# Kernel tuning notes

Measured on AMD Instinct MI355X. Metric: run time of the kernel, lower is better.

## Reference

```python
import jax, jax.numpy as jnp
import numpy as np

D_MODEL = 1024


def setup_inputs() -> dict:
    key = jax.random.key(0)
    ks = jax.random.split(key, 9)
    B, S, D = 4, 2048, D_MODEL
    scale = 1.0 / np.sqrt(D)
    inp = {
        "tokens": jax.random.normal(ks[0], (B, S, D), dtype=jnp.float32),
        "Wq": jax.random.normal(ks[1], (D, D), dtype=jnp.float32) * scale,
        "bq": jnp.zeros((D,), dtype=jnp.float32),
        "Wk": jax.random.normal(ks[2], (D, D), dtype=jnp.float32) * scale,
        "bk": jnp.zeros((D,), dtype=jnp.float32),
        "Wv": jax.random.normal(ks[3], (D, D), dtype=jnp.float32) * scale,
        "bv": jnp.zeros((D,), dtype=jnp.float32),
        "Wo": jax.random.normal(ks[4], (D, D), dtype=jnp.float32) * scale,
        "bo": jnp.zeros((D,), dtype=jnp.float32),
    }
    return inp


def reference(tokens, Wq, bq, Wk, bk, Wv, bv, Wo, bo):
    # use_activation=True, use_residual=True
    residual = tokens
    x = jax.nn.gelu(tokens, approximate=False)  # F.gelu default is exact (erf)
    q = jnp.einsum("bsd,de->bse", x, Wq) + bq
    k = jnp.einsum("bsd,de->bse", x, Wk) + bk
    v = jnp.einsum("bsd,de->bse", x, Wv) + bv
    scale = 1.0 / jnp.sqrt(jnp.asarray(tokens.shape[-1], dtype=tokens.dtype))
    scores = jnp.einsum("bqd,bkd->bqk", q, k) * scale  # [B,S,S]
    attn = jax.nn.softmax(scores, axis=-1)
    mixed = jnp.einsum("bqk,bkd->bqd", attn, v)
    out = jnp.einsum("bsd,de->bse", mixed, Wo) + bo
    return out + residual
```

## Files before the change

kernel.cpp:

```cpp
#include <hip/hip_runtime.h>
#include <hip/hip_bf16.h>
#include <cstdint>
#include <cstddef>

typedef unsigned short u16;
using frag_ab = __attribute__((ext_vector_type(8))) short;
using f32x4   = __attribute__((ext_vector_type(4))) float;

__device__ __forceinline__ u16 f2bf(float x) {
    __hip_bfloat16 h = __float2bfloat16(x);
    return *reinterpret_cast<u16*>(&h);
}

__device__ __forceinline__ void gload_lds16(const u16* g, u16* l) {
    __builtin_amdgcn_global_load_lds(
        (const __attribute__((address_space(1))) uint32_t*)g,
        (__attribute__((address_space(3)))       uint32_t*)l,
        16, 0, 0);
}

#define WAITV4() do { asm volatile("s_waitcnt vmcnt(4)" ::: "memory"); \
                      __builtin_amdgcn_sched_barrier(0); } while (0)
#define WAITV0() do { asm volatile("s_waitcnt vmcnt(0)" ::: "memory"); \
                      __builtin_amdgcn_sched_barrier(0); } while (0)
#define BAR()    do { asm volatile("" ::: "memory"); __builtin_amdgcn_s_barrier(); \
                      __builtin_amdgcn_sched_barrier(0); } while (0)
#define LGKMC(N) do { asm volatile("s_waitcnt lgkmcnt(" #N ")" ::: "memory"); \
                      __builtin_amdgcn_sched_barrier(0); } while (0)
#define LGKM0()  LGKMC(0)

template<int EPI, int BN_>
__global__ __launch_bounds__(512, 2)
void gemm8p(const u16* __restrict__ A, const u16* __restrict__ Bt,
            void* __restrict__ C0,
            const float* __restrict__ b0, const float* __restrict__ resid,
            int K, int lda, int ldb, int ldc,
            long long sA, long long sB, long long sC, float alpha,
            float* __restrict__ partials)
{
    constexpr int NFQ    = BN_ / 64;
    constexpr int WN     = BN_ / 2;
    constexpr int BUFSTR = 16384 + BN_ * 64;
    __shared__ __align__(16) u16 lds[2 * BUFSTR];

    const int z = blockIdx.z;
    A  += (long long)z * sA;
    Bt += (long long)z * sB;

    const int gx  = gridDim.x;
    const int nwg = gx * gridDim.y;
    const int cpx = nwg >> 3;
    int lin = blockIdx.x + gx * blockIdx.y;
    lin = (lin & 7) * cpx + (lin >> 3);
    const int m0 = (lin / gx) * 256;
    const int n0 = (lin % gx) * BN_;

    const int t    = threadIdx.x;
    const int lane = t & 63;
    const int wave = t >> 6;
    const int wm   = wave >> 1;
    const int wn   = wave & 1;

    const int r0  = t >> 3;
    const int ssw = (t & 7) ^ (r0 & 7);
    const u16* gsA0_0 = A  + (size_t)(m0 +       r0) * lda + ssw * 8;
    const u16* gsA0_1 = A  + (size_t)(m0 +  64 + r0) * lda + ssw * 8;
    const u16* gsA1_0 = A  + (size_t)(m0 + 128 + r0) * lda + ssw * 8;
    const u16* gsA1_1 = A  + (size_t)(m0 + 192 + r0) * lda + ssw * 8;
    const u16* gsB0_0 = Bt + (size_t)(n0 +       r0) * ldb + ssw * 8;
    const u16* gsB0_1 = Bt + (size_t)(n0 +  64 + r0) * ldb + ssw * 8;
    const u16* gsB1_0 = (BN_ == 256) ? Bt + (size_t)(n0 + 128 + r0) * ldb + ssw * 8 : gsB0_0;
    const u16* gsB1_1 = (BN_ == 256) ? Bt + (size_t)(n0 + 192 + r0) * ldb + ssw * 8 : gsB0_1;

#define OPO_A 0
#define OPO_B 16384
#define STAGE(BI, OP, H, KT) do {                                              \
    gload_lds16(gs##OP##H##_0 + (size_t)(KT) * 64,                             \
                lds + (BI) * BUFSTR + OPO_##OP + (H) * 8192 + t * 8);          \
    gload_lds16(gs##OP##H##_1 + (size_t)(KT) * 64,                             \
                lds + (BI) * BUFSTR + OPO_##OP + (H) * 8192 + 4096 + t * 8);   \
} while (0)

    const int ar   = lane & 15;
    const int ko   = lane >> 4;
    const int aoff = (wm * 64 + ar) * 64;
    const int boff = OPO_B + (wn * WN + ar) * 64;
    const int as0  = ((0 + ko) ^ (ar & 7)) * 8;
    const int as1  = ((4 + ko) ^ (ar & 7)) * 8;

    frag_ab areg[2][2];
    frag_ab breg[2][NFQ][2];
    f32x4   acc[4][2 * NFQ] = {};

#define RDA(BI, MQ) do { _Pragma("unroll") for (int mf = 0; mf < 2; ++mf) {    \
    areg[mf][0] = *(const frag_ab*)(lds + (BI)*BUFSTR + aoff + ((MQ)*2+mf)*1024 + as0); \
    areg[mf][1] = *(const frag_ab*)(lds + (BI)*BUFSTR + aoff + ((MQ)*2+mf)*1024 + as1); } } while (0)

#define RDB(BI, NQ) do { _Pragma("unroll") for (int jf = 0; jf < NFQ; ++jf) {  \
    breg[NQ][jf][0] = *(const frag_ab*)(lds + (BI)*BUFSTR + boff + ((NQ)*NFQ+jf)*1024 + as0); \
    breg[NQ][jf][1] = *(const frag_ab*)(lds + (BI)*BUFSTR + boff + ((NQ)*NFQ+jf)*1024 + as1); } } while (0)

#define MMAQ(MQ, NQ) do { __builtin_amdgcn_s_setprio(1);                       \
    _Pragma("unroll") for (int mf = 0; mf < 2; ++mf)                           \
    _Pragma("unroll") for (int jf = 0; jf < NFQ; ++jf) {                       \
        acc[(MQ)*2+mf][(NQ)*NFQ+jf] = __builtin_amdgcn_mfma_f32_16x16x32_bf16( \
            areg[mf][0], breg[NQ][jf][0], acc[(MQ)*2+mf][(NQ)*NFQ+jf], 0,0,0); \
        acc[(MQ)*2+mf][(NQ)*NFQ+jf] = __builtin_amdgcn_mfma_f32_16x16x32_bf16( \
            areg[mf][1], breg[NQ][jf][1], acc[(MQ)*2+mf][(NQ)*NFQ+jf], 0,0,0); \
    } __builtin_amdgcn_s_setprio(0); } while (0)

    const int nk = K / 64;
    STAGE(0, A, 0, 0); STAGE(0, A, 1, 0); STAGE(0, B, 0, 0);
    if constexpr (BN_ == 256) STAGE(0, B, 1, 0);
    STAGE(1, B, 0, 1); STAGE(1, A, 0, 1);
    WAITV4();
    BAR();

    const int nIter = nk >> 1;
    for (int it = 0; it < nIter; ++it) {
        const int O  = 2 * it + 1;
        const int E2 = (2 * it + 2 < nk) ? 2 * it + 2 : nk - 1;
        const int O2 = (2 * it + 3 < nk) ? 2 * it + 3 : nk - 1;

        RDA(0, 0); RDB(0, 0);
        STAGE(1, A, 1, O);
        if constexpr (BN_ == 256) LGKMC(8);
        BAR(); LGKM0(); MMAQ(0, 0);
        RDB(0, 1);
        if constexpr (BN_ == 256) STAGE(1, B, 1, O);
        BAR(); LGKM0(); MMAQ(0, 1);
        RDA(0, 1);
        STAGE(0, B, 0, E2);
        BAR(); LGKM0(); MMAQ(1, 0);
        STAGE(0, A, 0, E2);
        WAITV4();
        BAR(); MMAQ(1, 1);
        RDA(1, 0); RDB(1, 0);
        STAGE(0, A, 1, E2);
        if constexpr (BN_ == 256) LGKMC(8);
        BAR(); LGKM0(); MMAQ(0, 0);
        RDB(1, 1);
        if constexpr (BN_ == 256) STAGE(0, B, 1, E2);
        BAR(); LGKM0(); MMAQ(0, 1);
        RDA(1, 1);
        STAGE(1, B, 0, O2);
        BAR(); LGKM0(); MMAQ(1, 0);
        STAGE(1, A, 0, O2);
        WAITV4();
        BAR(); MMAQ(1, 1);
    }

    const int cr = (lane >> 4) * 4;
    const int cc = lane & 15;

    float* fl = (float*)lds;
    if constexpr (EPI == 2) {
        WAITV0();
        BAR();
        if (t < 256) {
            const float* p = partials + ((size_t)z * 2048 + m0 + t) * 16;
            float s = 0.0f;
            #pragma unroll
            for (int i = 0; i < 16; ++i) s += p[i];
            fl[t] = 1.0f / s;
        }
        BAR();
    }

    float rs[4][4];
    if constexpr (EPI == 1) {
        #pragma unroll
        for (int mi = 0; mi < 4; ++mi)
            #pragma unroll
            for (int r = 0; r < 4; ++r) rs[mi][r] = 0.0f;
    }

    #pragma unroll
    for (int mi = 0; mi < 4; ++mi) {
        const int rowb = m0 + wm * 64 + mi * 16 + cr;
        const int rloc = wm * 64 + mi * 16 + cr;
        #pragma unroll
        for (int gj = 0; gj < 2 * NFQ; ++gj) {
            const int col = n0 + wn * WN + gj * 16 + cc;
            const float bvv = (EPI == 3) ? b0[col] : 0.0f;
            #pragma unroll
            for (int r = 0; r < 4; ++r) {
                const size_t row = (size_t)(rowb + r);
                float v = acc[mi][gj][r];
                if (EPI == 1) { v = __expf(v * alpha); rs[mi][r] += v; }
                if (EPI == 2) v *= fl[rloc + r];
                v += bvv;
                if (EPI == 3) {
                    v += resid[row * ldc + col];
                    ((float*)C0)[(size_t)z * sC + row * ldc + col] = v;
                } else {
                    ((u16*)C0)[(size_t)z * sC + row * ldc + col] = f2bf(v);
                }
            }
        }
    }

    if constexpr (EPI == 1) {
        #pragma unroll
        for (int mi = 0; mi < 4; ++mi)
            #pragma unroll
            for (int r = 0; r < 4; ++r) {
                float s = rs[mi][r];
                s += __shfl_xor(s, 1); s += __shfl_xor(s, 2);
                s += __shfl_xor(s, 4); s += __shfl_xor(s, 8);
                rs[mi][r] = s;
            }
        if (cc == 0) {
            const int chunk = (n0 >> 7) + wn;
            #pragma unroll
            for (int mi = 0; mi < 4; ++mi) {
                const int rowb = m0 + wm * 64 + mi * 16 + cr;
                #pragma unroll
                for (int r = 0; r < 4; ++r)
                    partials[((size_t)z * 2048 + rowb + r) * 16 + chunk] = rs[mi][r];
            }
        }
    }
#undef STAGE
#undef RDA
#undef RDB
#undef MMAQ
#undef OPO_A
#undef OPO_B
}

__global__ __launch_bounds__(512, 2)
void gemmQK3(const u16* __restrict__ A, const u16* __restrict__ Bt,
             u16* __restrict__ C0, const float* __restrict__ b0,
             const float* __restrict__ b1,
             int K, int lda, int ldb, int ldc, long long sC)
{
    __shared__ __align__(16) u16 lds[81920];

    const int gx  = gridDim.x;
    const int nwg = gx * gridDim.y;
    const int cpx = nwg >> 3;
    int lin = blockIdx.x + gx * blockIdx.y;
    lin = (lin & 7) * cpx + (lin >> 3);
    const int m0 = (lin / gx) * 256;
    const int n0 = (lin % gx) * 256;

    const int t    = threadIdx.x;
    const int lane = t & 63;
    const int wave = t >> 6;
    const int wm   = wave >> 1;
    const int wn   = wave & 1;

    const int r0  = t >> 3;
    const int ssw = (t & 7) ^ (r0 & 7);
    const u16* gsA_0 = A  + (size_t)(m0 +       r0) * lda + ssw * 8;
    const u16* gsA_1 = A  + (size_t)(m0 +  64 + r0) * lda + ssw * 8;
    const u16* gsA_2 = A  + (size_t)(m0 + 128 + r0) * lda + ssw * 8;
    const u16* gsA_3 = A  + (size_t)(m0 + 192 + r0) * lda + ssw * 8;
    const u16* gsB_0 = Bt + (size_t)(n0 +       r0) * ldb + ssw * 8;
    const u16* gsB_1 = Bt + (size_t)(n0 +  64 + r0) * ldb + ssw * 8;
    const u16* gsB_2 = Bt + (size_t)(n0 + 128 + r0) * ldb + ssw * 8;
    const u16* gsB_3 = Bt + (size_t)(n0 + 192 + r0) * ldb + ssw * 8;

#define STA(BUF, H, KT) do {                                                   \
    gload_lds16(((H) ? gsA_2 : gsA_0) + (size_t)(KT) * 64,                     \
                lds + (BUF) * 16384 + (H) * 8192 + t * 8);                     \
    gload_lds16(((H) ? gsA_3 : gsA_1) + (size_t)(KT) * 64,                     \
                lds + (BUF) * 16384 + (H) * 8192 + 4096 + t * 8);              \
} while (0)
#define STB(BUF, H, KT) do {                                                   \
    gload_lds16(((H) ? gsB_2 : gsB_0) + (size_t)(KT) * 64,                     \
                lds + 49152 + (BUF) * 16384 + (H) * 8192 + t * 8);             \
    gload_lds16(((H) ? gsB_3 : gsB_1) + (size_t)(KT) * 64,                     \
                lds + 49152 + (BUF) * 16384 + (H) * 8192 + 4096 + t * 8);      \
} while (0)

    const int ar   = lane & 15;
    const int ko   = lane >> 4;
    const int aoff = (wm * 64 + ar) * 64;
    const int boff = 49152 + (wn * 128 + ar) * 64;
    const int as0  = ((0 + ko) ^ (ar & 7)) * 8;
    const int as1  = ((4 + ko) ^ (ar & 7)) * 8;

    frag_ab areg[2][2];
    frag_ab breg[2][4][2];
    f32x4   acc[4][8] = {};

#define RDA3(AB, MQ) do { _Pragma("unroll") for (int mf = 0; mf < 2; ++mf) {   \
    areg[mf][0] = *(const frag_ab*)(lds + (AB) + aoff + ((MQ)*2+mf)*1024 + as0); \
    areg[mf][1] = *(const frag_ab*)(lds + (AB) + aoff + ((MQ)*2+mf)*1024 + as1); } } while (0)

#define RDB3(BB, NQ) do { _Pragma("unroll") for (int jf = 0; jf < 4; ++jf) {   \
    breg[NQ][jf][0] = *(const frag_ab*)(lds + (BB) + boff + ((NQ)*4+jf)*1024 + as0); \
    breg[NQ][jf][1] = *(const frag_ab*)(lds + (BB) + boff + ((NQ)*4+jf)*1024 + as1); } } while (0)

#define MMAQ3(MQ, NQ) do { __builtin_amdgcn_s_setprio(1);                      \
    _Pragma("unroll") for (int mf = 0; mf < 2; ++mf)                           \
    _Pragma("unroll") for (int jf = 0; jf < 4; ++jf) {                         \
        acc[(MQ)*2+mf][(NQ)*4+jf] = __builtin_amdgcn_mfma_f32_16x16x32_bf16(   \
            areg[mf][0], breg[NQ][jf][0], acc[(MQ)*2+mf][(NQ)*4+jf], 0,0,0);   \
        acc[(MQ)*2+mf][(NQ)*4+jf] = __builtin_amdgcn_mfma_f32_16x16x32_bf16(   \
            areg[mf][1], breg[NQ][jf][1], acc[(MQ)*2+mf][(NQ)*4+jf], 0,0,0);   \
    } __builtin_amdgcn_s_setprio(0); } while (0)

    const int nk = K / 64;
    STA(0, 0, 0); STA(0, 1, 0);
    STB(0, 0, 0); STB(0, 1, 0);
    STA(1, 0, 1); STA(1, 1, 1);
    WAITV4();
    BAR();

    int ab = 0, bb = 0;
    for (int tt = 0; tt < nk; ++tt) {
        const int ab2 = (ab + 2 >= 3) ? ab - 1 : ab + 2;
        const int bb1 = bb ^ 1;
        const int tB  = (tt + 1 < nk) ? tt + 1 : nk - 1;
        const int tA  = (tt + 2 < nk) ? tt + 2 : nk - 1;
        const int AB = ab * 16384, BB = bb * 16384;
        RDA3(AB, 0); RDB3(BB, 0);
        STB(bb1, 0, tB);
        LGKMC(8);
        BAR(); LGKM0(); MMAQ3(0, 0);
        RDB3(BB, 1);
        STB(bb1, 1, tB);
        BAR(); LGKM0(); MMAQ3(0, 1);
        RDA3(AB, 1);
        STA(ab2, 0, tA);
        BAR(); LGKM0(); MMAQ3(1, 0);
        STA(ab2, 1, tA);
        WAITV4();
        BAR(); MMAQ3(1, 1);
        ab = (ab + 1 >= 3) ? 0 : ab + 1;
        bb = bb1;
    }

    const int cr = (lane >> 4) * 4;
    const int cc = lane & 15;
    #pragma unroll
    for (int mi = 0; mi < 4; ++mi) {
        const int rowb = m0 + wm * 64 + mi * 16 + cr;
        #pragma unroll
        for (int gj = 0; gj < 8; ++gj) {
            const int col = n0 + wn * 128 + gj * 16 + cc;
            const int plane = col >> 10;
            const int cl    = col & 1023;
            const float bvv = ((plane == 0) ? b0 : b1)[cl];
            u16* Cw = C0 + (size_t)plane * sC;
            #pragma unroll
            for (int r = 0; r < 4; ++r)
                Cw[(size_t)(rowb + r) * ldc + cl] = f2bf(acc[mi][gj][r] + bvv);
        }
    }
#undef STA
#undef STB
#undef RDA3
#undef RDB3
#undef MMAQ3
}

__global__ __launch_bounds__(256, 2)
void gemm128_v(const u16* __restrict__ A, const u16* __restrict__ Bt,
               u16* __restrict__ VT, const float* __restrict__ bv,
               int K, int lda, int ldb)
{
    constexpr int BUFSTR = 16384;
    __shared__ __align__(16) u16 lds[2 * BUFSTR];

    const int gx  = gridDim.x;
    const int nwg = gx * gridDim.y;
    const int cpx = nwg >> 3;
    int lin = blockIdx.x + gx * blockIdx.y;
    lin = (lin & 7) * cpx + (lin >> 3);
    const int m0 = (lin / gx) * 128;
    const int n0 = (lin % gx) * 128;

    const int t    = threadIdx.x;
    const int lane = t & 63;
    const int wave = t >> 6;
    const int wm   = wave >> 1;
    const int wn   = wave & 1;

    const int r0  = t >> 3;
    const int ssw = (t & 7) ^ (r0 & 7);
    const u16* gsA0_0 = A  + (size_t)(m0 +       r0) * lda + ssw * 8;
    const u16* gsA0_1 = A  + (size_t)(m0 +  32 + r0) * lda + ssw * 8;
    const u16* gsA1_0 = A  + (size_t)(m0 +  64 + r0) * lda + ssw * 8;
    const u16* gsA1_1 = A  + (size_t)(m0 +  96 + r0) * lda + ssw * 8;
    const u16* gsB0_0 = Bt + (size_t)(n0 +       r0) * ldb + ssw * 8;
    const u16* gsB0_1 = Bt + (size_t)(n0 +  32 + r0) * ldb + ssw * 8;
    const u16* gsB1_0 = Bt + (size_t)(n0 +  64 + r0) * ldb + ssw * 8;
    const u16* gsB1_1 = Bt + (size_t)(n0 +  96 + r0) * ldb + ssw * 8;

#define OPO_A 0
#define OPO_B 8192
#define STAGE(BI, OP, H, KT) do {                                              \
    gload_lds16(gs##OP##H##_0 + (size_t)(KT) * 64,                             \
                lds + (BI) * BUFSTR + OPO_##OP + (H) * 4096 + t * 8);          \
    gload_lds16(gs##OP##H##_1 + (size_t)(KT) * 64,                             \
                lds + (BI) * BUFSTR + OPO_##OP + (H) * 4096 + 2048 + t * 8);   \
} while (0)

    const int ar   = lane & 15;
    const int ko   = lane >> 4;
    const int aoff = (wm * 64 + ar) * 64;
    const int boff = OPO_B + (wn * 64 + ar) * 64;
    const int as0  = ((0 + ko) ^ (ar & 7)) * 8;
    const int as1  = ((4 + ko) ^ (ar & 7)) * 8;

    frag_ab areg[2][2];
    frag_ab breg[2][2][2];
    f32x4   acc[4][4] = {};

#define RDA(BI, MQ) do { _Pragma("unroll") for (int mf = 0; mf < 2; ++mf) {    \
    areg[mf][0] = *(const frag_ab*)(lds + (BI)*BUFSTR + aoff + ((MQ)*2+mf)*1024 + as0); \
    areg[mf][1] = *(const frag_ab*)(lds + (BI)*BUFSTR + aoff + ((MQ)*2+mf)*1024 + as1); } } while (0)

#define RDB(BI, NQ) do { _Pragma("unroll") for (int jf = 0; jf < 2; ++jf) {    \
    breg[NQ][jf][0] = *(const frag_ab*)(lds + (BI)*BUFSTR + boff + ((NQ)*2+jf)*1024 + as0); \
    breg[NQ][jf][1] = *(const frag_ab*)(lds + (BI)*BUFSTR + boff + ((NQ)*2+jf)*1024 + as1); } } while (0)

#define MMAQ(MQ, NQ) do { __builtin_amdgcn_s_setprio(1);                       \
    _Pragma("unroll") for (int mf = 0; mf < 2; ++mf)                           \
    _Pragma("unroll") for (int jf = 0; jf < 2; ++jf) {                         \
        acc[(MQ)*2+mf][(NQ)*2+jf] = __builtin_amdgcn_mfma_f32_16x16x32_bf16(   \
            areg[mf][0], breg[NQ][jf][0], acc[(MQ)*2+mf][(NQ)*2+jf], 0,0,0);   \
        acc[(MQ)*2+mf][(NQ)*2+jf] = __builtin_amdgcn_mfma_f32_16x16x32_bf16(   \
            areg[mf][1], breg[NQ][jf][1], acc[(MQ)*2+mf][(NQ)*2+jf], 0,0,0);   \
    } __builtin_amdgcn_s_setprio(0); } while (0)

    const int nk = K / 64;
    STAGE(0, A, 0, 0); STAGE(0, A, 1, 0); STAGE(0, B, 0, 0); STAGE(0, B, 1, 0);
    STAGE(1, B, 0, 1); STAGE(1, A, 0, 1);
    WAITV4();
    BAR();

    const int nIter = nk >> 1;
    for (int it = 0; it < nIter; ++it) {
        const int O  = 2 * it + 1;
        const int E2 = (2 * it + 2 < nk) ? 2 * it + 2 : nk - 1;
        const int O2 = (2 * it + 3 < nk) ? 2 * it + 3 : nk - 1;

        RDA(0, 0); RDB(0, 0); STAGE(1, A, 1, O);  BAR(); LGKM0(); MMAQ(0, 0);
        RDB(0, 1);            STAGE(1, B, 1, O);  BAR(); LGKM0(); MMAQ(0, 1);
        RDA(0, 1);            STAGE(0, B, 0, E2); BAR(); LGKM0(); MMAQ(1, 0);
        STAGE(0, A, 0, E2);   WAITV4();           BAR();          MMAQ(1, 1);
        RDA(1, 0); RDB(1, 0); STAGE(0, A, 1, E2); BAR(); LGKM0(); MMAQ(0, 0);
        RDB(1, 1);            STAGE(0, B, 1, E2); BAR(); LGKM0(); MMAQ(0, 1);
        RDA(1, 1);            STAGE(1, B, 0, O2); BAR(); LGKM0(); MMAQ(1, 0);
        STAGE(1, A, 0, O2);   WAITV4();           BAR();          MMAQ(1, 1);
    }

    const int cr = (lane >> 4) * 4;
    const int cc = lane & 15;

    WAITV0();
    BAR();
    constexpr int TP = 136;
    u16* T = lds;
    #pragma unroll
    for (int mi = 0; mi < 4; ++mi) {
        const int rloc = wm * 64 + mi * 16 + cr;
        #pragma unroll
        for (int gj = 0; gj < 4; ++gj) {
            const int cl = wn * 64 + gj * 16 + cc;
            const float bvv = bv[n0 + cl];
            union { u16 u[4]; uint2 q; } pk;
            #pragma unroll
            for (int r = 0; r < 4; ++r) pk.u[r] = f2bf(acc[mi][gj][r] + bvv);
            *(uint2*)&T[cl * TP + rloc] = pk.q;
        }
    }
    BAR();
    const int bb   = m0 >> 11;
    const int s0   = m0 & 2047;
    const int d    = t >> 1;
    const int half = t & 1;
    const u16* src = T + d * TP + half * 64;
    u16* dg = VT + (size_t)bb * 1024 * 2048 + (size_t)(n0 + d) * 2048 + s0 + half * 64;
    #pragma unroll
    for (int j = 0; j < 8; ++j)
        ((uint4*)dg)[j] = ((const uint4*)src)[j];
#undef STAGE
#undef RDA
#undef RDB
#undef MMAQ
#undef OPO_A
#undef OPO_B
}

__global__ __launch_bounds__(256)
void prep_kernel(const float4* __restrict__ in, uint4* __restrict__ outp,
                 const float* __restrict__ W0, const float* __restrict__ W1,
                 const float* __restrict__ W2, const float* __restrict__ W3,
                 u16* __restrict__ WT, int D, int NG)
{
    __shared__ float tile[32][33];
    const int b = blockIdx.x;
    const int t = threadIdx.x;
    if (b < NG) {
        const int i = (b * 256 + t) * 2;
        float4 x0 = in[i], x1 = in[i + 1];
        auto g = [](float v) { return 0.5f * v * (1.0f + erff(v * 0.70710678118654752f)); };
        union { u16 u[8]; uint4 q; } pk;
        pk.u[0] = f2bf(g(x0.x)); pk.u[1] = f2bf(g(x0.y));
        pk.u[2] = f2bf(g(x0.z)); pk.u[3] = f2bf(g(x0.w));
        pk.u[4] = f2bf(g(x1.x)); pk.u[5] = f2bf(g(x1.y));
        pk.u[6] = f2bf(g(x1.z)); pk.u[7] = f2bf(g(x1.w));
        outp[b * 256 + t] = pk.q;
        return;
    }
    const int j   = b - NG;
    const int z   = j >> 10;
    const int rem = j & 1023;
    const int n0  = (rem & 31) * 32;
    const int k0  = (rem >> 5) * 32;
    const float* W = (z == 0) ? W0 : (z == 1) ? W1 : (z == 2) ? W2 : W3;
    u16* o = WT + (size_t)z * D * D;
    const int tx = t & 31, ty = t >> 5;
    #pragma unroll
    for (int r = 0; r < 4; ++r)
        tile[ty + 8 * r][tx] = W[(size_t)(k0 + ty + 8 * r) * D + n0 + tx];
    __syncthreads();
    #pragma unroll
    for (int r = 0; r < 4; ++r)
        o[(size_t)(n0 + ty + 8 * r) * D + k0 + tx] = f2bf(tile[tx][ty + 8 * r]);
}

extern "C" void kernel_launch(void* const* d_in, const int* in_sizes, int n_in,
                              void* d_out, int out_size, void* d_ws, size_t ws_size,
                              hipStream_t stream)
{
    const int B = 4, S = 2048, D = 1024;
    const int M = B * S;

    const float* tokens = (const float*)d_in[0];
    const float* Wq = (const float*)d_in[1];
    const float* bq = (const float*)d_in[2];
    const float* Wk = (const float*)d_in[3];
    const float* bk = (const float*)d_in[4];
    const float* Wv = (const float*)d_in[5];
    const float* bv = (const float*)d_in[6];
    const float* Wo = (const float*)d_in[7];
    const float* bo = (const float*)d_in[8];
    float* out = (float*)d_out;

    char* ws = (char*)d_ws;
    size_t o = 0;
    u16* x_bf = (u16*)(ws + o); o += (size_t)M * D * 2;
    u16* wT   = (u16*)(ws + o); o += (size_t)4 * D * D * 2;
    u16* q_bf = (u16*)(ws + o); o += (size_t)M * D * 2;
    u16* k_bf = (u16*)(ws + o); o += (size_t)M * D * 2;
    u16* vt   = (u16*)(ws + o); o += (size_t)M * D * 2;
    u16*   E        = (u16*)(ws + o);   o += (size_t)B * S * S * 2;
    float* partials = (float*)(ws + o); o += (size_t)B * S * 16 * 4;
    u16* mixed = x_bf;

    const int NG = M * D / 8 / 256;
    prep_kernel<<<dim3(NG + 4096), dim3(256), 0, stream>>>(
        (const float4*)tokens, (uint4*)x_bf, Wq, Wk, Wv, Wo, wT, D, NG);

    gemmQK3<<<dim3(2 * D / 256, M / 256, 1), dim3(512), 0, stream>>>(
        x_bf, wT, q_bf, bq, bk, D, D, D, D, (long long)M * D);

    gemm128_v<<<dim3(D / 128, M / 128, 1), dim3(256), 0, stream>>>(
        x_bf, wT + 2 * D * D, vt, bv, D, D, D);

    gemm8p<1, 256><<<dim3(S / 256, S / 256, B), dim3(512), 0, stream>>>(
        q_bf, k_bf, E, nullptr, nullptr,
        D, D, D, S, (long long)S * D, (long long)S * D, (long long)S * S, 0.03125f,
        partials);

    gemm8p<2, 128><<<dim3(D / 128, S / 256, B), dim3(512), 0, stream>>>(
        E, vt, mixed, nullptr, nullptr,
        S, S, S, D, (long long)S * S, (long long)D * S, (long long)S * D, 1.0f,
        partials);

    gemm8p<3, 128><<<dim3(D / 128, M / 256, 1), dim3(512), 0, stream>>>(
        mixed, wT + 3 * D * D, out, bo, tokens,
        D, D, D, D, 0, 0, 0, 1.0f, nullptr);
}
```

Measured before the change: 168.3 us.

## Unify GEMMs on triple-buffered A / double-buffered B pipeline kernel

Replaces the double-buffered gemm8p main loop with the gemmQK3-style schedule, which uses three A buffers and two B buffers so A tiles are prefetched two k-steps ahead. The QK projection, the scores GEMM, the PV GEMM and the output projection all use this one templated kernel, with the QK bias split handled as a new epilogue mode. This aims to hide more global load latency per k-step. The cost is more LDS per block, which may reduce occupancy, particularly for the BN=256 variants. The weight transpose in prep also now writes packed 32-bit pairs instead of 16-bit scalars, for wider coalesced stores.

```diff
diff --git a/kernel.cpp b/kernel.cpp
--- a/kernel.cpp
+++ b/kernel.cpp
@@ -31,17 +31,17 @@
 
 template<int EPI, int BN_>
 __global__ __launch_bounds__(512, 2)
-void gemm8p(const u16* __restrict__ A, const u16* __restrict__ Bt,
+void gemm3a(const u16* __restrict__ A, const u16* __restrict__ Bt,
             void* __restrict__ C0,
             const float* __restrict__ b0, const float* __restrict__ resid,
             int K, int lda, int ldb, int ldc,
             long long sA, long long sB, long long sC, float alpha,
             float* __restrict__ partials)
 {
-    constexpr int NFQ    = BN_ / 64;
-    constexpr int WN     = BN_ / 2;
-    constexpr int BUFSTR = 16384 + BN_ * 64;
-    __shared__ __align__(16) u16 lds[2 * BUFSTR];
+    constexpr int NFQ  = BN_ / 64;
+    constexpr int WN   = BN_ / 2;
+    constexpr int BBUF = BN_ * 64;
+    __shared__ __align__(16) u16 lds[49152 + 2 * BBUF];
 
     const int z = blockIdx.z;
     A  += (long long)z * sA;
@@ -63,28 +63,32 @@
 
     const int r0  = t >> 3;
     const int ssw = (t & 7) ^ (r0 & 7);
-    const u16* gsA0_0 = A  + (size_t)(m0 +       r0) * lda + ssw * 8;
-    const u16* gsA0_1 = A  + (size_t)(m0 +  64 + r0) * lda + ssw * 8;
-    const u16* gsA1_0 = A  + (size_t)(m0 + 128 + r0) * lda + ssw * 8;
-    const u16* gsA1_1 = A  + (size_t)(m0 + 192 + r0) * lda + ssw * 8;
-    const u16* gsB0_0 = Bt + (size_t)(n0 +       r0) * ldb + ssw * 8;
-    const u16* gsB0_1 = Bt + (size_t)(n0 +  64 + r0) * ldb + ssw * 8;
-    const u16* gsB1_0 = (BN_ == 256) ? Bt + (size_t)(n0 + 128 + r0) * ldb + ssw * 8 : gsB0_0;
-    const u16* gsB1_1 = (BN_ == 256) ? Bt + (size_t)(n0 + 192 + r0) * ldb + ssw * 8 : gsB0_1;
-
-#define OPO_A 0
-#define OPO_B 16384
-#define STAGE(BI, OP, H, KT) do {                                              \
-    gload_lds16(gs##OP##H##_0 + (size_t)(KT) * 64,                             \
-                lds + (BI) * BUFSTR + OPO_##OP + (H) * 8192 + t * 8);          \
-    gload_lds16(gs##OP##H##_1 + (size_t)(KT) * 64,                             \
-                lds + (BI) * BUFSTR + OPO_##OP + (H) * 8192 + 4096 + t * 8);   \
+    const u16* gsA_0 = A  + (size_t)(m0 +       r0) * lda + ssw * 8;
+    const u16* gsA_1 = A  + (size_t)(m0 +  64 + r0) * lda + ssw * 8;
+    const u16* gsA_2 = A  + (size_t)(m0 + 128 + r0) * lda + ssw * 8;
+    const u16* gsA_3 = A  + (size_t)(m0 + 192 + r0) * lda + ssw * 8;
+    const u16* gsB_0 = Bt + (size_t)(n0 +       r0) * ldb + ssw * 8;
+    const u16* gsB_1 = Bt + (size_t)(n0 +  64 + r0) * ldb + ssw * 8;
+    const u16* gsB_2 = (BN_ == 256) ? Bt + (size_t)(n0 + 128 + r0) * ldb + ssw * 8 : gsB_0;
+    const u16* gsB_3 = (BN_ == 256) ? Bt + (size_t)(n0 + 192 + r0) * ldb + ssw * 8 : gsB_1;
+
+#define STA(BUF, H, KT) do {                                                   \
+    gload_lds16(((H) ? gsA_2 : gsA_0) + (size_t)(KT) * 64,                     \
+                lds + (BUF) * 16384 + (H) * 8192 + t * 8);                     \
+    gload_lds16(((H) ? gsA_3 : gsA_1) + (size_t)(KT) * 64,                     \
+                lds + (BUF) * 16384 + (H) * 8192 + 4096 + t * 8);              \
+} while (0)
+#define STB(BUF, H, KT) do {                                                   \
+    gload_lds16(((H) ? gsB_2 : gsB_0) + (size_t)(KT) * 64,                     \
+                lds + 49152 + (BUF) * BBUF + (H) * 8192 + t * 8);              \
+    gload_lds16(((H) ? gsB_3 : gsB_1) + (size_t)(KT) * 64,                     \
+                lds + 49152 + (BUF) * BBUF + (H) * 8192 + 4096 + t * 8);       \
 } while (0)
 
     const int ar   = lane & 15;
     const int ko   = lane >> 4;
     const int aoff = (wm * 64 + ar) * 64;
-    const int boff = OPO_B + (wn * WN + ar) * 64;
+    const int boff = 49152 + (wn * WN + ar) * 64;
     const int as0  = ((0 + ko) ^ (ar & 7)) * 8;
     const int as1  = ((4 + ko) ^ (ar & 7)) * 8;
 
@@ -92,15 +96,15 @@
     frag_ab breg[2][NFQ][2];
     f32x4   acc[4][2 * NFQ] = {};
 
-#define RDA(BI, MQ) do { _Pragma("unroll") for (int mf = 0; mf < 2; ++mf) {    \
-    areg[mf][0] = *(const frag_ab*)(lds + (BI)*BUFSTR + aoff + ((MQ)*2+mf)*1024 + as0); \
-    areg[mf][1] = *(const frag_ab*)(lds + (BI)*BUFSTR + aoff + ((MQ)*2+mf)*1024 + as1); } } while (0)
-
-#define RDB(BI, NQ) do { _Pragma("unroll") for (int jf = 0; jf < NFQ; ++jf) {  \
-    breg[NQ][jf][0] = *(const frag_ab*)(lds + (BI)*BUFSTR + boff + ((NQ)*NFQ+jf)*1024 + as0); \
-    breg[NQ][jf][1] = *(const frag_ab*)(lds + (BI)*BUFSTR + boff + ((NQ)*NFQ+jf)*1024 + as1); } } while (0)
-
-#define MMAQ(MQ, NQ) do { __builtin_amdgcn_s_setprio(1);                       \
+#define RDA3(AB, MQ) do { _Pragma("unroll") for (int mf = 0; mf < 2; ++mf) {   \
+    areg[mf][0] = *(const frag_ab*)(lds + (AB) + aoff + ((MQ)*2+mf)*1024 + as0); \
+    areg[mf][1] = *(const frag_ab*)(lds + (AB) + aoff + ((MQ)*2+mf)*1024 + as1); } } while (0)
+
+#define RDB3(BO, NQ) do { _Pragma("unroll") for (int jf = 0; jf < NFQ; ++jf) { \
+    breg[NQ][jf][0] = *(const frag_ab*)(lds + (BO) + boff + ((NQ)*NFQ+jf)*1024 + as0); \
+    breg[NQ][jf][1] = *(const frag_ab*)(lds + (BO) + boff + ((NQ)*NFQ+jf)*1024 + as1); } } while (0)
+
+#define MMAQ3(MQ, NQ) do { __builtin_amdgcn_s_setprio(1);                      \
     _Pragma("unroll") for (int mf = 0; mf < 2; ++mf)                           \
     _Pragma("unroll") for (int jf = 0; jf < NFQ; ++jf) {                       \
         acc[(MQ)*2+mf][(NQ)*NFQ+jf] = __builtin_amdgcn_mfma_f32_16x16x32_bf16( \
@@ -110,44 +114,35 @@
     } __builtin_amdgcn_s_setprio(0); } while (0)
 
     const int nk = K / 64;
-    STAGE(0, A, 0, 0); STAGE(0, A, 1, 0); STAGE(0, B, 0, 0);
-    if constexpr (BN_ == 256) STAGE(0, B, 1, 0);
-    STAGE(1, B, 0, 1); STAGE(1, A, 0, 1);
+    STA(0, 0, 0); STA(0, 1, 0);
+    STB(0, 0, 0);
+    if constexpr (BN_ == 256) STB(0, 1, 0);
+    STA(1, 0, 1); STA(1, 1, 1);
     WAITV4();
     BAR();
 
-    const int nIter = nk >> 1;
-    for (int it = 0; it < nIter; ++it) {
-        const int O  = 2 * it + 1;
-        const int E2 = (2 * it + 2 < nk) ? 2 * it + 2 : nk - 1;
-        const int O2 = (2 * it + 3 < nk) ? 2 * it + 3 : nk - 1;
-
-        RDA(0, 0); RDB(0, 0);
-        STAGE(1, A, 1, O);
+    int ab = 0, bb = 0;
+    for (int tt = 0; tt < nk; ++tt) {
+        const int ab2 = (ab + 2 >= 3) ? ab - 1 : ab + 2;
+        const int bb1 = bb ^ 1;
+        const int tB  = (tt + 1 < nk) ? tt + 1 : nk - 1;
+        const int tA  = (tt + 2 < nk) ? tt + 2 : nk - 1;
+        const int AB = ab * 16384, BB = bb * BBUF;
+        RDA3(AB, 0); RDB3(BB, 0);
+        STB(bb1, 0, tB);
         if constexpr (BN_ == 256) LGKMC(8);
-        BAR(); LGKM0(); MMAQ(0, 0);
-        RDB(0, 1);
-        if constexpr (BN_ == 256) STAGE(1, B, 1, O);
-        BAR(); LGKM0(); MMAQ(0, 1);
-        RDA(0, 1);
-        STAGE(0, B, 0, E2);
-        BAR(); LGKM0(); MMAQ(1, 0);
-        STAGE(0, A, 0, E2);
+        BAR(); LGKM0(); MMAQ3(0, 0);
+        RDB3(BB, 1);
+        if constexpr (BN_ == 256) STB(bb1, 1, tB);
+        BAR(); LGKM0(); MMAQ3(0, 1);
+        RDA3(AB, 1);
+        STA(ab2, 0, tA);
+        BAR(); LGKM0(); MMAQ3(1, 0);
+        STA(ab2, 1, tA);
         WAITV4();
-        BAR(); MMAQ(1, 1);
-        RDA(1, 0); RDB(1, 0);
-        STAGE(0, A, 1, E2);
-        if constexpr (BN_ == 256) LGKMC(8);
-        BAR(); LGKM0(); MMAQ(0, 0);
-        RDB(1, 1);
-        if constexpr (BN_ == 256) STAGE(0, B, 1, E2);
-        BAR(); LGKM0(); MMAQ(0, 1);
-        RDA(1, 1);
-        STAGE(1, B, 0, O2);
-        BAR(); LGKM0(); MMAQ(1, 0);
-        STAGE(1, A, 0, O2);
-        WAITV4();
-        BAR(); MMAQ(1, 1);
+        BAR(); MMAQ3(1, 1);
+        ab = (ab + 1 >= 3) ? 0 : ab + 1;
+        bb = bb1;
     }
 
     const int cr = (lane >> 4) * 4;
@@ -182,19 +177,29 @@
         #pragma unroll
         for (int gj = 0; gj < 2 * NFQ; ++gj) {
             const int col = n0 + wn * WN + gj * 16 + cc;
-            const float bvv = (EPI == 3) ? b0[col] : 0.0f;
-            #pragma unroll
-            for (int r = 0; r < 4; ++r) {
-                const size_t row = (size_t)(rowb + r);
-                float v = acc[mi][gj][r];
-                if (EPI == 1) { v = __expf(v * alpha); rs[mi][r] += v; }
-                if (EPI == 2) v *= fl[rloc + r];
-                v += bvv;
-                if (EPI == 3) {
-                    v += resid[row * ldc + col];
-                    ((float*)C0)[(size_t)z * sC + row * ldc + col] = v;
-                } else {
-                    ((u16*)C0)[(size_t)z * sC + row * ldc + col] = f2bf(v);
+            if constexpr (EPI == 0) {
+                const int plane = col >> 10;
+                const int cl    = col & 1023;
+                const float bvv = ((plane == 0) ? b0 : resid)[cl];
+                u16* Cw = (u16*)C0 + (size_t)plane * sC;
+                #pragma unroll
+                for (int r = 0; r < 4; ++r)
+                    Cw[(size_t)(rowb + r) * ldc + cl] = f2bf(acc[mi][gj][r] + bvv);
+            } else {
+                const float bvv = (EPI == 3) ? b0[col] : 0.0f;
+                #pragma unroll
+                for (int r = 0; r < 4; ++r) {
+                    const size_t row = (size_t)(rowb + r);
+                    float v = acc[mi][gj][r];
+                    if (EPI == 1) { v = __expf(v * alpha); rs[mi][r] += v; }
+                    if (EPI == 2) v *= fl[rloc + r];
+                    v += bvv;
+                    if (EPI == 3) {
+                        v += resid[row * ldc + col];
+                        ((float*)C0)[(size_t)z * sC + row * ldc + col] = v;
+                    } else {
+                        ((u16*)C0)[(size_t)z * sC + row * ldc + col] = f2bf(v);
+                    }
                 }
             }
         }
@@ -221,136 +226,6 @@
             }
         }
     }
-#undef STAGE
-#undef RDA
-#undef RDB
-#undef MMAQ
-#undef OPO_A
-#undef OPO_B
-}
-
-__global__ __launch_bounds__(512, 2)
-void gemmQK3(const u16* __restrict__ A, const u16* __restrict__ Bt,
-             u16* __restrict__ C0, const float* __restrict__ b0,
-             const float* __restrict__ b1,
-             int K, int lda, int ldb, int ldc, long long sC)
-{
-    __shared__ __align__(16) u16 lds[81920];
-
-    const int gx  = gridDim.x;
-    const int nwg = gx * gridDim.y;
-    const int cpx = nwg >> 3;
-    int lin = blockIdx.x + gx * blockIdx.y;
-    lin = (lin & 7) * cpx + (lin >> 3);
-    const int m0 = (lin / gx) * 256;
-    const int n0 = (lin % gx) * 256;
-
-    const int t    = threadIdx.x;
-    const int lane = t & 63;
-    const int wave = t >> 6;
-    const int wm   = wave >> 1;
-    const int wn   = wave & 1;
-
-    const int r0  = t >> 3;
-    const int ssw = (t & 7) ^ (r0 & 7);
-    const u16* gsA_0 = A  + (size_t)(m0 +       r0) * lda + ssw * 8;
-    const u16* gsA_1 = A  + (size_t)(m0 +  64 + r0) * lda + ssw * 8;
-    const u16* gsA_2 = A  + (size_t)(m0 + 128 + r0) * lda + ssw * 8;
-    const u16* gsA_3 = A  + (size_t)(m0 + 192 + r0) * lda + ssw * 8;
-    const u16* gsB_0 = Bt + (size_t)(n0 +       r0) * ldb + ssw * 8;
-    const u16* gsB_1 = Bt + (size_t)(n0 +  64 + r0) * ldb + ssw * 8;
-    const u16* gsB_2 = Bt + (size_t)(n0 + 128 + r0) * ldb + ssw * 8;
-    const u16* gsB_3 = Bt + (size_t)(n0 + 192 + r0) * ldb + ssw * 8;
-
-#define STA(BUF, H, KT) do {                                                   \
-    gload_lds16(((H) ? gsA_2 : gsA_0) + (size_t)(KT) * 64,                     \
-                lds + (BUF) * 16384 + (H) * 8192 + t * 8);                     \
-    gload_lds16(((H) ? gsA_3 : gsA_1) + (size_t)(KT) * 64,                     \
-                lds + (BUF) * 16384 + (H) * 8192 + 4096 + t * 8);              \
-} while (0)
-#define STB(BUF, H, KT) do {                                                   \
-    gload_lds16(((H) ? gsB_2 : gsB_0) + (size_t)(KT) * 64,                     \
-                lds + 49152 + (BUF) * 16384 + (H) * 8192 + t * 8);             \
-    gload_lds16(((H) ? gsB_3 : gsB_1) + (size_t)(KT) * 64,                     \
-                lds + 49152 + (BUF) * 16384 + (H) * 8192 + 4096 + t * 8);      \
-} while (0)
-
-    const int ar   = lane & 15;
-    const int ko   = lane >> 4;
-    const int aoff = (wm * 64 + ar) * 64;
-    const int boff = 49152 + (wn * 128 + ar) * 64;
-    const int as0  = ((0 + ko) ^ (ar & 7)) * 8;
-    const int as1  = ((4 + ko) ^ (ar & 7)) * 8;
-
-    frag_ab areg[2][2];
-    frag_ab breg[2][4][2];
-    f32x4   acc[4][8] = {};
-
-#define RDA3(AB, MQ) do { _Pragma("unroll") for (int mf = 0; mf < 2; ++mf) {   \
-    areg[mf][0] = *(const frag_ab*)(lds + (AB) + aoff + ((MQ)*2+mf)*1024 + as0); \
-    areg[mf][1] = *(const frag_ab*)(lds + (AB) + aoff + ((MQ)*2+mf)*1024 + as1); } } while (0)
-
-#define RDB3(BB, NQ) do { _Pragma("unroll") for (int jf = 0; jf < 4; ++jf) {   \
-    breg[NQ][jf][0] = *(const frag_ab*)(lds + (BB) + boff + ((NQ)*4+jf)*1024 + as0); \
-    breg[NQ][jf][1] = *(const frag_ab*)(lds + (BB) + boff + ((NQ)*4+jf)*1024 + as1); } } while (0)
-
-#define MMAQ3(MQ, NQ) do { __builtin_amdgcn_s_setprio(1);                      \
-    _Pragma("unroll") for (int mf = 0; mf < 2; ++mf)                           \
-    _Pragma("unroll") for (int jf = 0; jf < 4; ++jf) {                         \
-        acc[(MQ)*2+mf][(NQ)*4+jf] = __builtin_amdgcn_mfma_f32_16x16x32_bf16(   \
-            areg[mf][0], breg[NQ][jf][0], acc[(MQ)*2+mf][(NQ)*4+jf], 0,0,0);   \
-        acc[(MQ)*2+mf][(NQ)*4+jf] = __builtin_amdgcn_mfma_f32_16x16x32_bf16(   \
-            areg[mf][1], breg[NQ][jf][1], acc[(MQ)*2+mf][(NQ)*4+jf], 0,0,0);   \
-    } __builtin_amdgcn_s_setprio(0); } while (0)
-
-    const int nk = K / 64;
-    STA(0, 0, 0); STA(0, 1, 0);
-    STB(0, 0, 0); STB(0, 1, 0);
-    STA(1, 0, 1); STA(1, 1, 1);
-    WAITV4();
-    BAR();
-
-    int ab = 0, bb = 0;
-    for (int tt = 0; tt < nk; ++tt) {
-        const int ab2 = (ab + 2 >= 3) ? ab - 1 : ab + 2;
-        const int bb1 = bb ^ 1;
-        const int tB  = (tt + 1 < nk) ? tt + 1 : nk - 1;
-        const int tA  = (tt + 2 < nk) ? tt + 2 : nk - 1;
-        const int AB = ab * 16384, BB = bb * 16384;
-        RDA3(AB, 0); RDB3(BB, 0);
-        STB(bb1, 0, tB);
-        LGKMC(8);
-        BAR(); LGKM0(); MMAQ3(0, 0);
-        RDB3(BB, 1);
-        STB(bb1, 1, tB);
-        BAR(); LGKM0(); MMAQ3(0, 1);
-        RDA3(AB, 1);
-        STA(ab2, 0, tA);
-        BAR(); LGKM0(); MMAQ3(1, 0);
-        STA(ab2, 1, tA);
-        WAITV4();
-        BAR(); MMAQ3(1, 1);
-        ab = (ab + 1 >= 3) ? 0 : ab + 1;
-        bb = bb1;
-    }
-
-    const int cr = (lane >> 4) * 4;
-    const int cc = lane & 15;
-    #pragma unroll
-    for (int mi = 0; mi < 4; ++mi) {
-        const int rowb = m0 + wm * 64 + mi * 16 + cr;
-        #pragma unroll
-        for (int gj = 0; gj < 8; ++gj) {
-            const int col = n0 + wn * 128 + gj * 16 + cc;
-            const int plane = col >> 10;
-            const int cl    = col & 1023;
-            const float bvv = ((plane == 0) ? b0 : b1)[cl];
-            u16* Cw = C0 + (size_t)plane * sC;
-            #pragma unroll
-            for (int r = 0; r < 4; ++r)
-                Cw[(size_t)(rowb + r) * ldc + cl] = f2bf(acc[mi][gj][r] + bvv);
-        }
-    }
 #undef STA
 #undef STB
 #undef RDA3
@@ -521,9 +396,15 @@
     for (int r = 0; r < 4; ++r)
         tile[ty + 8 * r][tx] = W[(size_t)(k0 + ty + 8 * r) * D + n0 + tx];
     __syncthreads();
+    const int tx16 = t & 15, ny = t >> 4;
     #pragma unroll
-    for (int r = 0; r < 4; ++r)
-        o[(size_t)(n0 + ty + 8 * r) * D + k0 + tx] = f2bf(tile[tx][ty + 8 * r]);
+    for (int r = 0; r < 2; ++r) {
+        const int nl = ny + 16 * r;
+        union { u16 u[2]; unsigned q; } pk;
+        pk.u[0] = f2bf(tile[2 * tx16][nl]);
+        pk.u[1] = f2bf(tile[2 * tx16 + 1][nl]);
+        ((unsigned*)(o + (size_t)(n0 + nl) * D + k0))[tx16] = pk.q;
+    }
 }
 
 extern "C" void kernel_launch(void* const* d_in, const int* in_sizes, int n_in,
@@ -559,23 +440,24 @@
     prep_kernel<<<dim3(NG + 4096), dim3(256), 0, stream>>>(
         (const float4*)tokens, (uint4*)x_bf, Wq, Wk, Wv, Wo, wT, D, NG);
 
-    gemmQK3<<<dim3(2 * D / 256, M / 256, 1), dim3(512), 0, stream>>>(
-        x_bf, wT, q_bf, bq, bk, D, D, D, D, (long long)M * D);
+    gemm3a<0, 256><<<dim3(2 * D / 256, M / 256, 1), dim3(512), 0, stream>>>(
+        x_bf, wT, q_bf, bq, bk,
+        D, D, D, D, 0, 0, (long long)M * D, 1.0f, nullptr);
 
     gemm128_v<<<dim3(D / 128, M / 128, 1), dim3(256), 0, stream>>>(
         x_bf, wT + 2 * D * D, vt, bv, D, D, D);
 
-    gemm8p<1, 256><<<dim3(S / 256, S / 256, B), dim3(512), 0, stream>>>(
+    gemm3a<1, 256><<<dim3(S / 256, S / 256, B), dim3(512), 0, stream>>>(
         q_bf, k_bf, E, nullptr, nullptr,
         D, D, D, S, (long long)S * D, (long long)S * D, (long long)S * S, 0.03125f,
         partials);
 
-    gemm8p<2, 128><<<dim3(D / 128, S / 256, B), dim3(512), 0, stream>>>(
+    gemm3a<2, 128><<<dim3(D / 128, S / 256, B), dim3(512), 0, stream>>>(
         E, vt, mixed, nullptr, nullptr,
         S, S, S, D, (long long)S * S, (long long)D * S, (long long)S * D, 1.0f,
         partials);
 
-    gemm8p<3, 128><<<dim3(D / 128, M / 256, 1), dim3(512), 0, stream>>>(
+    gemm3a<3, 128><<<dim3(D / 128, M / 256, 1), dim3(512), 0, stream>>>(
         mixed, wT + 3 * D * D, out, bo, tokens,
         D, D, D, D, 0, 0, 0, 1.0f, nullptr);
 }
```

After: 167.4 us. Within noise of the previous version (-0.5%).
